# Performance work log

Hardware: AMD Instinct MI355X
Metric: run time of the kernel (lower is better)

Reference implementation:

```python
import jax, jax.numpy as jnp
import numpy as np

RADIUS = 0.08       # float radius -> patches_radius float branch
K = 32              # patch_size_source; spacing = 0 so topk k == K


def setup_inputs() -> dict:
    key = jax.random.key(0)
    k1, k2, k3, k4 = jax.random.split(key, 4)
    B, Ns, Nt = 2, 2048, 32768  # Nt = 32**3 (perfect cube for H_t reshape)
    return {
        "source": jax.random.normal(k1, (B, Ns, 3), dtype=jnp.float32),
        "target": jax.random.normal(k2, (B, Nt, 3), dtype=jnp.float32),
        "source_density": jax.random.uniform(k3, (B, Ns, 1), dtype=jnp.float32),
        "target_density": jax.random.uniform(k4, (B, Nt, 1), dtype=jnp.float32),
    }


def reference(source, target, source_density, target_density):
    B, Ns, _ = source.shape
    Nt = target.shape[1]

    # pairwise squared distances: (B, Nt, Ns)
    r0 = jnp.sum(target * target, axis=2, keepdims=True)            # B,Nt,1
    r1 = jnp.sum(source * source, axis=2, keepdims=True)            # B,Ns,1
    sq_dist = r0 - 2.0 * jnp.einsum('btc,bsc->bts', target, source) + jnp.swapaxes(r1, 1, 2)

    # computed in the original forward but never used downstream (dead value)
    _sq_dist_sel = sq_dist / (jnp.einsum('bti,bsi->bts', target_density, source_density) + 1e-8)

    # top-k nearest neighbors (spacing == 0)
    neg_vals, idx = jax.lax.top_k(-sq_dist, K)                      # B,Nt,K
    sq_pd = -neg_vals

    rad = RADIUS * jnp.ones((B, 1, 1), dtype=sq_dist.dtype)
    valid = (rad ** 2) >= sq_pd                                     # B,Nt,K (rad broadcast)
    idx = jnp.where(valid, idx, -1)

    b_idx = jnp.arange(B)[:, None, None]                            # B,1,1
    src_s = source / (rad + 1e-6)
    tgt_s = target / (rad + 1e-6)

    safe = jnp.maximum(idx, 0)
    patches = jnp.where(valid[..., None], src_s[b_idx, safe], 0.0)  # B,Nt,K,3
    patches = patches - tgt_s[:, :, None, :]
    density = jnp.where(valid[..., None], source_density[b_idx, safe], 0.0)  # B,Nt,K,1

    # gather of an all-ones (B,Ns) mask == validity indicator
    patch_valid = valid.astype(patches.dtype)
    patches_size = jnp.sum(patch_valid, axis=-1)                    # B,Nt

    patches_dist = jnp.sqrt(jnp.maximum(sq_pd, 1e-9)) / (rad + 1e-6)  # B,Nt,K

    mask_cnt = jnp.sum((idx < 0).astype(jnp.int32), axis=-1, keepdims=True)  # B,Nt,1
    weight_density = jnp.sum(density, axis=-2) / mask_cnt            # B,Nt,1

    H = int(round(Nt ** (1.0 / 3.0)))
    patches_idx = jnp.stack([jnp.broadcast_to(b_idx, (B, Nt, K)), idx], axis=-1)

    return (
        patches.reshape(B, H, H, H, K, 3),        # patches source
        patches_idx.reshape(B, H, H, H, K, 2),    # patches idx source
        patches_size,                              # patches size source
        rad,                                       # patches radius source
        patches_dist.reshape(B, H, H, H, K),       # patches dist source
        weight_density,                            # weighted density
    )
```

## Files before the change

### kernel.cpp

```cpp
#include <hip/hip_runtime.h>
#include <math.h>

constexpr int B_  = 2;
constexpr int NS_ = 2048;
constexpr int NT_ = 32768;
constexpr int K_  = 32;
#define RADIUS_F 0.08f

constexpr int TPB = 512;
constexpr int WAVES = TPB / 64;
constexpr int TGT_PER_WAVE = 8;
constexpr int TGT_PER_BLOCK = WAVES * TGT_PER_WAVE;
constexpr int BLOCKS_PER_BATCH = NT_ / TGT_PER_BLOCK;
constexpr int NCHUNK = NS_ / 64;

constexpr long long SZ_PATCH = (long long)B_ * NT_ * K_ * 3;
constexpr long long SZ_IDX   = (long long)B_ * NT_ * K_ * 2;
constexpr long long SZ_SIZE  = (long long)B_ * NT_;
constexpr long long SZ_RAD   = B_;
constexpr long long SZ_DIST  = (long long)B_ * NT_ * K_;
constexpr long long O_PATCH = 0;
constexpr long long O_IDX   = O_PATCH + SZ_PATCH;
constexpr long long O_SIZE  = O_IDX + SZ_IDX;
constexpr long long O_RAD   = O_SIZE + SZ_SIZE;
constexpr long long O_DIST  = O_RAD + SZ_RAD;
constexpr long long O_WD    = O_DIST + SZ_DIST;

constexpr unsigned long long tm_mask(int k, int j) {
    unsigned long long m = 0;
    for (int l = 0; l < 64; ++l)
        if (((l & k) == 0) == ((l & j) == 0)) m |= 1ull << l;
    return m;
}

__device__ __forceinline__ float readlane_f(float v, int l) {
    return __int_as_float(__builtin_amdgcn_readlane(__float_as_int(v), l));
}
__device__ __forceinline__ float bperm_f(int addr, float v) {
    return __int_as_float(__builtin_amdgcn_ds_bpermute(addr, __float_as_int(v)));
}
__device__ __forceinline__ float shr1_f(float v) {
    return __int_as_float(__builtin_amdgcn_update_dpp(0, __float_as_int(v),
                                                      0x138, 0xF, 0xF, true));
}
__device__ __forceinline__ float med3_vsv(float pv, int vbits, float lv) {
    float r;
    asm("v_med3_f32 %0, %1, %2, %3" : "=v"(r) : "v"(pv), "s"(vbits), "v"(lv));
    return r;
}
__device__ __forceinline__ void cnds(float& lv, float pv, unsigned long long keep) {
    float r;
    asm("v_cndmask_b32 %0, %2, %1, %3" : "=v"(r) : "v"(lv), "v"(pv), "s"(keep));
    lv = r;
}
__device__ __forceinline__ float dist_f(float tx, float ty, float tz, float r0, float4 sp) {
    float dot = __fadd_rn(__fadd_rn(__fmul_rn(tx, sp.x), __fmul_rn(ty, sp.y)), __fmul_rn(tz, sp.z));
    return __fadd_rn(__fsub_rn(r0, __fmul_rn(2.0f, dot)), sp.w);
}

#define BSTG(LV, AJ, K, J) { \
    constexpr unsigned long long tm_ = tm_mask(K, J); \
    float pv_ = bperm_f(AJ, LV); \
    unsigned long long sm_ = __ballot((LV) < pv_); \
    cnds(LV, pv_, ~(sm_ ^ tm_)); \
}
#define BSTG2(AJ, K, J) { BSTG(lv0, AJ, K, J) BSTG(lv1, AJ, K, J) }

#define INS_LOOP(D, LV, T, RV, RI, NV, BASE) { \
    unsigned long long m_ = __ballot((D) < (T)); \
    while (m_) { \
        const int sl_ = (int)__builtin_ctzll(m_); m_ &= m_ - 1; \
        const int vb_ = __builtin_amdgcn_readlane(__float_as_int(D), sl_); \
        if (vb_ <= r2i) { \
            if (lane == (NV)) { RV = __int_as_float(vb_); RI = (BASE) + sl_; } \
            ++(NV); \
        } \
        LV = med3_vsv(shr1_f(LV), vb_, LV); \
    } \
}

__device__ __forceinline__ void epilogue(
    float* __restrict__ out, const float* __restrict__ sden, const float4* ssp,
    int b, long long tb, int lane,
    float lv, float rv, int ri, int nv,
    float tx, float ty, float tz)
{
    const float invdd = 1.0f / (RADIUS_F + 1e-6f);
    int vflag = 0; int vidx = -1; float dsum = 0.f; int vcnt = 0;
    const long long sdb = (long long)b * NS_;
    const int nvc = (nv > 64) ? 64 : nv;
    for (int s = 0; s < nvc; ++s) {
        float vr = readlane_f(rv, s);
        int   ir = __builtin_amdgcn_readlane(ri, s);
        int rank = (int)__popcll(__ballot(lv < vr));
        for (int q = 0; q < s; ++q)
            rank += (readlane_f(rv, q) == vr) ? 1 : 0;
        if (rank < K_) {
            dsum += sden[sdb + ir];
            ++vcnt;
            if (lane == rank) { vflag = 1; vidx = ir; }
        }
    }
    float px = 0.f, py = 0.f, pz = 0.f;
    if (vflag) { float4 spv = ssp[vidx]; px = spv.x; py = spv.y; pz = spv.z; }
    const float tsx = tx * invdd, tsy = ty * invdd, tsz = tz * invdd;
    if (lane < K_) {
        const long long pb = tb * K_ + lane;
        float3 p3;
        p3.x = (vflag ? px * invdd : 0.0f) - tsx;
        p3.y = (vflag ? py * invdd : 0.0f) - tsy;
        p3.z = (vflag ? pz * invdd : 0.0f) - tsz;
        *reinterpret_cast<float3*>(&out[O_PATCH + pb * 3]) = p3;
        float2 ix;
        ix.x = (float)b;
        ix.y = (float)vidx;
        *reinterpret_cast<float2*>(&out[O_IDX + pb * 2]) = ix;
        out[O_DIST + tb * K_ + lane] = sqrtf(fmaxf(lv, 1e-9f)) * invdd;
    }
    if (lane == 0) {
        out[O_SIZE + tb] = (float)vcnt;
        out[O_WD + tb]   = dsum / (float)(K_ - vcnt);
    }
}

__global__ __launch_bounds__(TPB, 8) void group_points_kernel(
    const float* __restrict__ src,
    const float* __restrict__ tgt,
    const float* __restrict__ sden,
    float* __restrict__ out)
{
    __shared__ float4 s_sp[NS_];

    const int tid  = threadIdx.x;
    const int lane = tid & 63;
    const int wav  = tid >> 6;
    const int b    = blockIdx.x / BLOCKS_PER_BATCH;
    const int tile = blockIdx.x % BLOCKS_PER_BATCH;

    for (int j = tid; j < NS_; j += TPB) {
        const float* p = src + ((long long)b * NS_ + j) * 3;
        float x = p[0], y = p[1], z = p[2];
        float r1 = __fadd_rn(__fadd_rn(__fmul_rn(x, x), __fmul_rn(y, y)), __fmul_rn(z, z));
        s_sp[j] = make_float4(x, y, z, r1);
    }
    if (blockIdx.x == 0 && tid == 0) {
        out[O_RAD + 0] = RADIUS_F;
        out[O_RAD + 1] = RADIUS_F;
    }
    __syncthreads();

    const float r2f = __fmul_rn(RADIUS_F, RADIUS_F);
    const int   r2i = __float_as_int(r2f);
    const int a1  = (lane ^ 1)  << 2;
    const int a2  = (lane ^ 2)  << 2;
    const int a4  = (lane ^ 4)  << 2;
    const int a8  = (lane ^ 8)  << 2;
    const int a16 = (lane ^ 16) << 2;
    const int a32 = (lane ^ 32) << 2;

    for (int gp = 0; gp < TGT_PER_WAVE / 2; ++gp) {
        const int t0 = tile * TGT_PER_BLOCK + wav * TGT_PER_WAVE + 2 * gp;
        const long long tb0 = (long long)b * NT_ + t0;
        const float* tp = tgt + tb0 * 3;
        const float tx0 = tp[0], ty0 = tp[1], tz0 = tp[2];
        const float tx1 = tp[3], ty1 = tp[4], tz1 = tp[5];
        const float r00 = __fadd_rn(__fadd_rn(__fmul_rn(tx0, tx0), __fmul_rn(ty0, ty0)), __fmul_rn(tz0, tz0));
        const float r01 = __fadd_rn(__fadd_rn(__fmul_rn(tx1, tx1), __fmul_rn(ty1, ty1)), __fmul_rn(tz1, tz1));

        float rv0 = 0.f, rv1 = 0.f; int ri0 = 0, ri1 = 0; int nv0 = 0, nv1 = 0;

        float lv0, lv1;
        {
            float4 sp = s_sp[lane];
            float d0 = dist_f(tx0, ty0, tz0, r00, sp);
            float d1 = dist_f(tx1, ty1, tz1, r01, sp);
            unsigned long long mr0 = __ballot(r2f >= d0);
            while (mr0) {
                int sl = (int)__builtin_ctzll(mr0); mr0 &= mr0 - 1;
                float v = readlane_f(d0, sl);
                if (lane == nv0) { rv0 = v; ri0 = sl; }
                ++nv0;
            }
            unsigned long long mr1 = __ballot(r2f >= d1);
            while (mr1) {
                int sl = (int)__builtin_ctzll(mr1); mr1 &= mr1 - 1;
                float v = readlane_f(d1, sl);
                if (lane == nv1) { rv1 = v; ri1 = sl; }
                ++nv1;
            }
            lv0 = d0; lv1 = d1;
        }
        BSTG2(a1, 2, 1)
        BSTG2(a2, 4, 2)  BSTG2(a1, 4, 1)
        BSTG2(a4, 8, 4)  BSTG2(a2, 8, 2)  BSTG2(a1, 8, 1)
        BSTG2(a8, 16, 8) BSTG2(a4, 16, 4) BSTG2(a2, 16, 2) BSTG2(a1, 16, 1)
        BSTG2(a16, 32, 16) BSTG2(a8, 32, 8) BSTG2(a4, 32, 4) BSTG2(a2, 32, 2) BSTG2(a1, 32, 1)
        BSTG2(a32, 64, 32) BSTG2(a16, 64, 16) BSTG2(a8, 64, 8) BSTG2(a4, 64, 4) BSTG2(a2, 64, 2) BSTG2(a1, 64, 1)
        float T0 = readlane_f(lv0, 31);
        float T1 = readlane_f(lv1, 31);

        for (int c = 1; c < NCHUNK; ++c) {
            float4 sp = s_sp[(c << 6) + lane];
            float d0 = dist_f(tx0, ty0, tz0, r00, sp);
            float d1 = dist_f(tx1, ty1, tz1, r01, sp);
            const int base = c << 6;
            INS_LOOP(d0, lv0, T0, rv0, ri0, nv0, base)
            INS_LOOP(d1, lv1, T1, rv1, ri1, nv1, base)
            T0 = readlane_f(lv0, 31);
            T1 = readlane_f(lv1, 31);
        }

        epilogue(out, sden, s_sp, b, tb0,     lane, lv0, rv0, ri0, nv0, tx0, ty0, tz0);
        epilogue(out, sden, s_sp, b, tb0 + 1, lane, lv1, rv1, ri1, nv1, tx1, ty1, tz1);
    }
}

extern "C" void kernel_launch(void* const* d_in, const int* in_sizes, int n_in,
                              void* d_out, int out_size, void* d_ws, size_t ws_size,
                              hipStream_t stream) {
    const float* src  = (const float*)d_in[0];
    const float* tgt  = (const float*)d_in[1];
    const float* sden = (const float*)d_in[2];
    float* out = (float*)d_out;

    dim3 grid(B_ * BLOCKS_PER_BATCH);
    group_points_kernel<<<grid, TPB, 0, stream>>>(src, tgt, sden, out);
}
```

Baseline: 216.0 us.

## Process four targets per wave, seed with 128-point bitonic merge, pairwise insertion

After: 209.3 us. -3.1%, faster.

```diff
diff --git a/kernel.cpp b/kernel.cpp
--- a/kernel.cpp
+++ b/kernel.cpp
@@ -8,9 +8,8 @@
 #define RADIUS_F 0.08f
 
 constexpr int TPB = 512;
-constexpr int WAVES = TPB / 64;
 constexpr int TGT_PER_WAVE = 8;
-constexpr int TGT_PER_BLOCK = WAVES * TGT_PER_WAVE;
+constexpr int TGT_PER_BLOCK = 8 * TGT_PER_WAVE;
 constexpr int BLOCKS_PER_BATCH = NT_ / TGT_PER_BLOCK;
 constexpr int NCHUNK = NS_ / 64;
 
@@ -48,6 +47,16 @@
     asm("v_med3_f32 %0, %1, %2, %3" : "=v"(r) : "v"(pv), "s"(vbits), "v"(lv));
     return r;
 }
+__device__ __forceinline__ float maxs_f(float p, int wbits) {
+    float r;
+    asm("v_max_f32 %0, %1, %2" : "=v"(r) : "s"(wbits), "v"(p));
+    return r;
+}
+__device__ __forceinline__ float min3_f(float a, float b, float c) {
+    float r;
+    asm("v_min3_f32 %0, %1, %2, %3" : "=v"(r) : "v"(a), "v"(b), "v"(c));
+    return r;
+}
 __device__ __forceinline__ void cnds(float& lv, float pv, unsigned long long keep) {
     float r;
     asm("v_cndmask_b32 %0, %2, %1, %3" : "=v"(r) : "v"(lv), "v"(pv), "s"(keep));
@@ -64,18 +73,38 @@
     unsigned long long sm_ = __ballot((LV) < pv_); \
     cnds(LV, pv_, ~(sm_ ^ tm_)); \
 }
-#define BSTG2(AJ, K, J) { BSTG(lv0, AJ, K, J) BSTG(lv1, AJ, K, J) }
-
-#define INS_LOOP(D, LV, T, RV, RI, NV, BASE) { \
+#define S8(AJ, K, J) { BSTG(sa0, AJ, K, J) BSTG(sa1, AJ, K, J) BSTG(sa2, AJ, K, J) BSTG(sa3, AJ, K, J) \
+                       BSTG(sb0, AJ, K, J) BSTG(sb1, AJ, K, J) BSTG(sb2, AJ, K, J) BSTG(sb3, AJ, K, J) }
+#define C4(AJ, J) { BSTG(sa0, AJ, 128, J) BSTG(sa1, AJ, 128, J) BSTG(sa2, AJ, 128, J) BSTG(sa3, AJ, 128, J) }
+
+#define REC(D, RV, RI, NV, BASE) { \
+    unsigned long long mr_ = __ballot(r2f >= (D)); \
+    while (mr_) { \
+        int sl_ = (int)__builtin_ctzll(mr_); mr_ &= mr_ - 1; \
+        float v_ = readlane_f(D, sl_); \
+        if (lane == (NV)) { RV = v_; RI = (BASE) + sl_; } \
+        ++(NV); \
+    } \
+}
+
+#define INS2(D, LV, T) { \
     unsigned long long m_ = __ballot((D) < (T)); \
     while (m_) { \
-        const int sl_ = (int)__builtin_ctzll(m_); m_ &= m_ - 1; \
-        const int vb_ = __builtin_amdgcn_readlane(__float_as_int(D), sl_); \
-        if (vb_ <= r2i) { \
-            if (lane == (NV)) { RV = __int_as_float(vb_); RI = (BASE) + sl_; } \
-            ++(NV); \
+        const int sl1_ = (int)__builtin_ctzll(m_); m_ &= m_ - 1; \
+        const int b1_ = __builtin_amdgcn_readlane(__float_as_int(D), sl1_); \
+        if (m_) { \
+            const int sl2_ = (int)__builtin_ctzll(m_); m_ &= m_ - 1; \
+            const int b2_ = __builtin_amdgcn_readlane(__float_as_int(D), sl2_); \
+            const int w1_ = (b1_ < b2_) ? b1_ : b2_; \
+            const int w2_ = (b1_ < b2_) ? b2_ : b1_; \
+            float p1_ = shr1_f(LV); \
+            float p2_ = shr1_f(p1_); \
+            float t1_ = maxs_f(p1_, w1_); \
+            float t2_ = maxs_f(p2_, w2_); \
+            LV = min3_f(LV, t1_, t2_); \
+        } else { \
+            LV = med3_vsv(shr1_f(LV), b1_, LV); \
         } \
-        LV = med3_vsv(shr1_f(LV), vb_, LV); \
     } \
 }
 
@@ -150,68 +179,82 @@
     __syncthreads();
 
     const float r2f = __fmul_rn(RADIUS_F, RADIUS_F);
-    const int   r2i = __float_as_int(r2f);
     const int a1  = (lane ^ 1)  << 2;
     const int a2  = (lane ^ 2)  << 2;
     const int a4  = (lane ^ 4)  << 2;
     const int a8  = (lane ^ 8)  << 2;
     const int a16 = (lane ^ 16) << 2;
     const int a32 = (lane ^ 32) << 2;
-
-    for (int gp = 0; gp < TGT_PER_WAVE / 2; ++gp) {
-        const int t0 = tile * TGT_PER_BLOCK + wav * TGT_PER_WAVE + 2 * gp;
+    const int arev = (63 - lane) << 2;
+
+    for (int gp = 0; gp < TGT_PER_WAVE / 4; ++gp) {
+        const int t0 = tile * TGT_PER_BLOCK + wav * TGT_PER_WAVE + gp * 4;
         const long long tb0 = (long long)b * NT_ + t0;
         const float* tp = tgt + tb0 * 3;
-        const float tx0 = tp[0], ty0 = tp[1], tz0 = tp[2];
-        const float tx1 = tp[3], ty1 = tp[4], tz1 = tp[5];
+        const float tx0 = tp[0],  ty0 = tp[1],  tz0 = tp[2];
+        const float tx1 = tp[3],  ty1 = tp[4],  tz1 = tp[5];
+        const float tx2 = tp[6],  ty2 = tp[7],  tz2 = tp[8];
+        const float tx3 = tp[9],  ty3 = tp[10], tz3 = tp[11];
         const float r00 = __fadd_rn(__fadd_rn(__fmul_rn(tx0, tx0), __fmul_rn(ty0, ty0)), __fmul_rn(tz0, tz0));
         const float r01 = __fadd_rn(__fadd_rn(__fmul_rn(tx1, tx1), __fmul_rn(ty1, ty1)), __fmul_rn(tz1, tz1));
-
-        float rv0 = 0.f, rv1 = 0.f; int ri0 = 0, ri1 = 0; int nv0 = 0, nv1 = 0;
-
-        float lv0, lv1;
-        {
-            float4 sp = s_sp[lane];
-            float d0 = dist_f(tx0, ty0, tz0, r00, sp);
-            float d1 = dist_f(tx1, ty1, tz1, r01, sp);
-            unsigned long long mr0 = __ballot(r2f >= d0);
-            while (mr0) {
-                int sl = (int)__builtin_ctzll(mr0); mr0 &= mr0 - 1;
-                float v = readlane_f(d0, sl);
-                if (lane == nv0) { rv0 = v; ri0 = sl; }
-                ++nv0;
-            }
-            unsigned long long mr1 = __ballot(r2f >= d1);
-            while (mr1) {
-                int sl = (int)__builtin_ctzll(mr1); mr1 &= mr1 - 1;
-                float v = readlane_f(d1, sl);
-                if (lane == nv1) { rv1 = v; ri1 = sl; }
-                ++nv1;
-            }
-            lv0 = d0; lv1 = d1;
-        }
-        BSTG2(a1, 2, 1)
-        BSTG2(a2, 4, 2)  BSTG2(a1, 4, 1)
-        BSTG2(a4, 8, 4)  BSTG2(a2, 8, 2)  BSTG2(a1, 8, 1)
-        BSTG2(a8, 16, 8) BSTG2(a4, 16, 4) BSTG2(a2, 16, 2) BSTG2(a1, 16, 1)
-        BSTG2(a16, 32, 16) BSTG2(a8, 32, 8) BSTG2(a4, 32, 4) BSTG2(a2, 32, 2) BSTG2(a1, 32, 1)
-        BSTG2(a32, 64, 32) BSTG2(a16, 64, 16) BSTG2(a8, 64, 8) BSTG2(a4, 64, 4) BSTG2(a2, 64, 2) BSTG2(a1, 64, 1)
-        float T0 = readlane_f(lv0, 31);
-        float T1 = readlane_f(lv1, 31);
-
-        for (int c = 1; c < NCHUNK; ++c) {
+        const float r02 = __fadd_rn(__fadd_rn(__fmul_rn(tx2, tx2), __fmul_rn(ty2, ty2)), __fmul_rn(tz2, tz2));
+        const float r03 = __fadd_rn(__fadd_rn(__fmul_rn(tx3, tx3), __fmul_rn(ty3, ty3)), __fmul_rn(tz3, tz3));
+
+        float rv0 = 0.f, rv1 = 0.f, rv2 = 0.f, rv3 = 0.f;
+        int   ri0 = 0,   ri1 = 0,   ri2 = 0,   ri3 = 0;
+        int   nv0 = 0,   nv1 = 0,   nv2 = 0,   nv3 = 0;
+
+        float4 sp0 = s_sp[lane];
+        float4 sp1 = s_sp[64 + lane];
+        float sa0 = dist_f(tx0, ty0, tz0, r00, sp0);
+        float sa1 = dist_f(tx1, ty1, tz1, r01, sp0);
+        float sa2 = dist_f(tx2, ty2, tz2, r02, sp0);
+        float sa3 = dist_f(tx3, ty3, tz3, r03, sp0);
+        float sb0 = dist_f(tx0, ty0, tz0, r00, sp1);
+        float sb1 = dist_f(tx1, ty1, tz1, r01, sp1);
+        float sb2 = dist_f(tx2, ty2, tz2, r02, sp1);
+        float sb3 = dist_f(tx3, ty3, tz3, r03, sp1);
+        REC(sa0, rv0, ri0, nv0, 0)  REC(sb0, rv0, ri0, nv0, 64)
+        REC(sa1, rv1, ri1, nv1, 0)  REC(sb1, rv1, ri1, nv1, 64)
+        REC(sa2, rv2, ri2, nv2, 0)  REC(sb2, rv2, ri2, nv2, 64)
+        REC(sa3, rv3, ri3, nv3, 0)  REC(sb3, rv3, ri3, nv3, 64)
+        S8(a1, 2, 1)
+        S8(a2, 4, 2)   S8(a1, 4, 1)
+        S8(a4, 8, 4)   S8(a2, 8, 2)   S8(a1, 8, 1)
+        S8(a8, 16, 8)  S8(a4, 16, 4)  S8(a2, 16, 2)  S8(a1, 16, 1)
+        S8(a16, 32, 16) S8(a8, 32, 8) S8(a4, 32, 4)  S8(a2, 32, 2)  S8(a1, 32, 1)
+        S8(a32, 64, 32) S8(a16, 64, 16) S8(a8, 64, 8) S8(a4, 64, 4) S8(a2, 64, 2) S8(a1, 64, 1)
+        sa0 = fminf(sa0, bperm_f(arev, sb0));
+        sa1 = fminf(sa1, bperm_f(arev, sb1));
+        sa2 = fminf(sa2, bperm_f(arev, sb2));
+        sa3 = fminf(sa3, bperm_f(arev, sb3));
+        C4(a32, 32) C4(a16, 16) C4(a8, 8) C4(a4, 4) C4(a2, 2) C4(a1, 1)
+        float T0 = readlane_f(sa0, 31);
+        float T1 = readlane_f(sa1, 31);
+        float T2 = readlane_f(sa2, 31);
+        float T3 = readlane_f(sa3, 31);
+
+        for (int c = 2; c < NCHUNK; ++c) {
             float4 sp = s_sp[(c << 6) + lane];
             float d0 = dist_f(tx0, ty0, tz0, r00, sp);
             float d1 = dist_f(tx1, ty1, tz1, r01, sp);
+            float d2 = dist_f(tx2, ty2, tz2, r02, sp);
+            float d3 = dist_f(tx3, ty3, tz3, r03, sp);
             const int base = c << 6;
-            INS_LOOP(d0, lv0, T0, rv0, ri0, nv0, base)
-            INS_LOOP(d1, lv1, T1, rv1, ri1, nv1, base)
-            T0 = readlane_f(lv0, 31);
-            T1 = readlane_f(lv1, 31);
+            REC(d0, rv0, ri0, nv0, base)
+            REC(d1, rv1, ri1, nv1, base)
+            REC(d2, rv2, ri2, nv2, base)
+            REC(d3, rv3, ri3, nv3, base)
+            INS2(d0, sa0, T0)  T0 = readlane_f(sa0, 31);
+            INS2(d1, sa1, T1)  T1 = readlane_f(sa1, 31);
+            INS2(d2, sa2, T2)  T2 = readlane_f(sa2, 31);
+            INS2(d3, sa3, T3)  T3 = readlane_f(sa3, 31);
         }
 
-        epilogue(out, sden, s_sp, b, tb0,     lane, lv0, rv0, ri0, nv0, tx0, ty0, tz0);
-        epilogue(out, sden, s_sp, b, tb0 + 1, lane, lv1, rv1, ri1, nv1, tx1, ty1, tz1);
+        epilogue(out, sden, s_sp, b, tb0,     lane, sa0, rv0, ri0, nv0, tx0, ty0, tz0);
+        epilogue(out, sden, s_sp, b, tb0 + 1, lane, sa1, rv1, ri1, nv1, tx1, ty1, tz1);
+        epilogue(out, sden, s_sp, b, tb0 + 2, lane, sa2, rv2, ri2, nv2, tx2, ty2, tz2);
+        epilogue(out, sden, s_sp, b, tb0 + 3, lane, sa3, rv3, ri3, nv3, tx3, ty3, tz3);
     }
 }
 
```
